# Kernel optimization log

Measured on AMD Instinct MI355X. Metric: run time of the kernel, lower is better.

## Reference

```python
import jax, jax.numpy as jnp
import numpy as np
from jax import lax

BETA = 10.0  # undeclared global softmax temperature in the source
STRIDE = 1
PADDING = 1


def setup_inputs() -> dict:
    key = jax.random.key(0)
    k1, k2 = jax.random.split(key)
    B, Ci, Co, K, L = 32, 256, 256, 3, 7  # num_level_conv=8 -> L=7
    x = jax.random.normal(k1, (B, Ci, 56, 56), dtype=jnp.float32)
    p_c = jax.random.normal(k2, (Co, Ci, K, K, L), dtype=jnp.float32)
    # reset_parameters with num_level=8, s=1: t1=4, t2=floor(log2(1))=0,
    # t3=arange(-2,1)=[-2,-1,0] -> q_level = sort(-2**t3) ++ [0] ++ 2**t3
    t3 = np.arange(-2, 1, dtype=np.float32)
    q_level = jnp.asarray(
        np.concatenate([np.sort(-(2.0 ** t3)), np.zeros(1, np.float32), 2.0 ** t3]),
        dtype=jnp.float32,
    )
    return {"x": x, "p_c": p_c, "q_level": q_level}


def reference(x, p_c, q_level):
    # soft quantization of the conv weight
    norm = jnp.sqrt(jnp.sum(p_c * p_c, axis=-1, keepdims=True))  # (O,I,K,K,1)
    s_c = jax.nn.softmax(BETA * (p_c / norm), axis=-1)           # (O,I,K,K,L)
    conv_w = jnp.einsum("oihwl,l->oihw", s_c, q_level)           # (O,I,K,K)
    # the source's double loop over (kh,kw) with strided slicing + matmul
    # is exactly stride-S cross-correlation with zero padding
    out = lax.conv_general_dilated(
        x,
        conv_w,
        window_strides=(STRIDE, STRIDE),
        padding=[(PADDING, PADDING), (PADDING, PADDING)],
        dimension_numbers=("NCHW", "OIHW", "NCHW"),
    )
    return out
```

## Files before the change

### kernel.cpp

```cpp
#include <hip/hip_runtime.h>
#include <math.h>

#define CI   256
#define CO   256
#define HW   56
#define LQ   7
#define BETA 10.0f

typedef __attribute__((ext_vector_type(8)))  short short8;
typedef __attribute__((ext_vector_type(16))) float f32x16;
typedef __attribute__((ext_vector_type(4)))  float f32x4;

__device__ __forceinline__ ushort f2bf(float f) {
    uint u = __float_as_uint(f);
    u += 0x7FFF + ((u >> 16) & 1);
    return (ushort)(u >> 16);
}

__global__ __launch_bounds__(256) void quant_weights(const float* __restrict__ p_c,
                                                     const float* __restrict__ q_level,
                                                     short* __restrict__ W2) {
    int idx = blockIdx.x * 256 + threadIdx.x;
    if (idx >= CO * CI * 9) return;
    int coci = idx / 9;
    int t = idx - coci * 9;
    int co = coci >> 8, ci = coci & 255;
    const float* p = p_c + (size_t)idx * LQ;
    float pv[LQ];
    float ss = 0.f;
#pragma unroll
    for (int l = 0; l < LQ; ++l) { pv[l] = p[l]; ss += pv[l] * pv[l]; }
    float inv = rsqrtf(ss) * BETA;
    float m = -1e30f;
#pragma unroll
    for (int l = 0; l < LQ; ++l) { pv[l] *= inv; m = fmaxf(m, pv[l]); }
    float den = 0.f, num = 0.f;
#pragma unroll
    for (int l = 0; l < LQ; ++l) {
        float e = expf(pv[l] - m);
        den += e;
        num += e * q_level[l];
    }
    int widx = ((((ci >> 5) * 9 + t) * 4 + ((ci >> 3) & 3)) * 2048) + co * 8 + (ci & 7);
    W2[widx] = (short)f2bf(num / den);
}

__global__ __launch_bounds__(256) void prep_main(const float* __restrict__ x,
                                                 ushort* __restrict__ xt) {
    __shared__ ushort ld[256 * 60];
    const int tid = threadIdx.x;
    const int h = blockIdx.x;
    const int b = blockIdx.y;

    if (h == 0 || h == 55) {
        int rr = (h == 0) ? 0 : 57;
        size_t base = ((size_t)b * 58 + rr) * 58 * 256;
        uint4 z = {0, 0, 0, 0};
        for (int i = tid; i < 58 * 256 / 8; i += 256)
            *(uint4*)&xt[base + (size_t)i * 8] = z;
    }
    if (tid < 64) {
        int col = (tid >> 5) * 57;
        int chk = tid & 31;
        size_t o = (((size_t)b * 58 + h + 1) * 58 + col) * 256 + chk * 8;
        uint4 z = {0, 0, 0, 0};
        *(uint4*)&xt[o] = z;
    }

    const float* xp = x + ((size_t)b * CI) * 3136 + h * HW;
#pragma unroll
    for (int s = 0; s < 14; ++s) {
        int flat = s * 1024 + tid * 4;
        int ci = flat / 56;
        int w  = flat - ci * 56;
        const float4 v = *(const float4*)(xp + (size_t)ci * 3136 + w);
        ushort4 o;
        o.x = f2bf(v.x); o.y = f2bf(v.y); o.z = f2bf(v.z); o.w = f2bf(v.w);
        *(ushort4*)&ld[ci * 60 + w] = o;
    }
    __syncthreads();
    const int w = tid & 63;
    const int wq = tid >> 6;
    if (w < 56) {
        size_t obase = (((size_t)b * 58 + h + 1) * 58 + (w + 1)) * 256;
#pragma unroll
        for (int s = 0; s < 8; ++s) {
            int cig = s * 4 + wq;
            int base = (cig * 8) * 60 + w;
            uint u0 = (uint)ld[base]       | ((uint)ld[base + 60]  << 16);
            uint u1 = (uint)ld[base + 120] | ((uint)ld[base + 180] << 16);
            uint u2 = (uint)ld[base + 240] | ((uint)ld[base + 300] << 16);
            uint u3 = (uint)ld[base + 360] | ((uint)ld[base + 420] << 16);
            uint4 o = {u0, u1, u2, u3};
            *(uint4*)&xt[obase + cig * 8] = o;
        }
    }
}

__global__ __launch_bounds__(256, 3) void conv_mfma3(const ushort* __restrict__ xt_g,
                                                     const short* __restrict__ W2,
                                                     float* __restrict__ out) {
    __shared__ __align__(16) ushort xt[2][8448];

    const int tid  = threadIdx.x;
    const int lane = tid & 63;
    const int wv   = tid >> 6;
    const int l31  = lane & 31;
    const int hi   = lane >> 5;
    const int wm   = (wv >> 1) * 64;
    const int wn   = wv & 1;

    const int h0  = blockIdx.x * 2;
    const int co0 = blockIdx.y * 128;
    const int b   = blockIdx.z;

    int src_off[5];
#pragma unroll
    for (int s = 0; s < 5; ++s) {
        int gl = s * 64 + lane;
        int g  = wv * 264 + (gl < 264 ? gl : 0);
        int kbq = g & 3, pos = g >> 2;
        int r = pos / 66, c = pos - r * 66;
        int cc = c < 58 ? c : 57;
        int cig = kbq ^ ((c >> 1) & 3);
        src_off[s] = ((b * 58 + h0 + r) * 58 + cc) * 256 + cig * 8;
    }

    f32x16 acc[2][2];
#pragma unroll
    for (int a = 0; a < 2; ++a)
#pragma unroll
        for (int f = 0; f < 2; ++f)
#pragma unroll
            for (int j = 0; j < 16; ++j) acc[a][f][j] = 0.f;

#pragma unroll
    for (int s = 0; s < 5; ++s) {
        if (s * 64 + lane < 264)
            __builtin_amdgcn_global_load_lds(
                (const __attribute__((address_space(1))) void*)(xt_g + src_off[s]),
                (__attribute__((address_space(3))) void*)&xt[0][(wv * 264 + s * 64) * 8],
                16, 0, 0);
    }

    for (int ch = 0; ch < 8; ++ch) {
        if (ch < 7) {
            const ushort* sp = xt_g + (ch + 1) * 32;
#pragma unroll
            for (int s = 0; s < 5; ++s) {
                if (s * 64 + lane < 264)
                    __builtin_amdgcn_global_load_lds(
                        (const __attribute__((address_space(1))) void*)(sp + src_off[s]),
                        (__attribute__((address_space(3))) void*)&xt[(ch + 1) & 1][(wv * 264 + s * 64) * 8],
                        16, 0, 0);
            }
            asm volatile("s_waitcnt vmcnt(5)" ::: "memory");
        } else {
            asm volatile("s_waitcnt vmcnt(0)" ::: "memory");
        }
        __builtin_amdgcn_s_barrier();

        const ushort* buf = xt[ch & 1];
#pragma unroll
        for (int kh = 0; kh < 3; ++kh) {
#pragma unroll
            for (int kw = 0; kw < 3; ++kw) {
                const int t = kh * 3 + kw;
#pragma unroll
                for (int k2 = 0; k2 < 2; ++k2) {
                    const int kb = k2 * 2 + hi;
                    const short* ap = W2 + (size_t)(((ch * 9 + t) * 4 + kb) * 256 + co0 + wm + l31) * 8;
                    short8 a0 = *(const short8*)ap;
                    short8 a1 = *(const short8*)(ap + 32 * 8);

                    const int c  = kw + l31;
                    const int r  = wn + kh;
                    const ushort* bp = &buf[((r * 66 + c) * 4 + (kb ^ ((c >> 1) & 3))) * 8];
                    short8 b0 = *(const short8*)bp;
                    short8 b1 = *(const short8*)(bp + 32 * 4 * 8);

                    acc[0][0] = __builtin_amdgcn_mfma_f32_32x32x16_bf16(a0, b0, acc[0][0], 0, 0, 0);
                    acc[0][1] = __builtin_amdgcn_mfma_f32_32x32x16_bf16(a0, b1, acc[0][1], 0, 0, 0);
                    acc[1][0] = __builtin_amdgcn_mfma_f32_32x32x16_bf16(a1, b0, acc[1][0], 0, 0, 0);
                    acc[1][1] = __builtin_amdgcn_mfma_f32_32x32x16_bf16(a1, b1, acc[1][1], 0, 0, 0);
                }
            }
        }
        asm volatile("s_waitcnt lgkmcnt(0)" ::: "memory");
        __builtin_amdgcn_s_barrier();
    }

    const int h = h0 + wn;
#pragma unroll
    for (int a = 0; a < 2; ++a) {
#pragma unroll
        for (int f = 0; f < 2; ++f) {
            int w = f * 32 + l31;
            if (w < HW) {
#pragma unroll
                for (int j = 0; j < 16; ++j) {
                    int co = co0 + wm + a * 32 + (j & 3) + 8 * (j >> 2) + 4 * hi;
                    out[(((size_t)b * CO + co) * HW + h) * HW + w] = acc[a][f][j];
                }
            }
        }
    }
}

__global__ __launch_bounds__(256, 2) void conv_mfma_fb(const float* __restrict__ x,
                                                       const short* __restrict__ W2,
                                                       float* __restrict__ out) {
    __shared__ __align__(16) short xs[6 * 72 * 32];

    const int tid  = threadIdx.x;
    const int lane = tid & 63;
    const int wv   = tid >> 6;
    const int l15  = lane & 15;
    const int kb   = lane >> 4;
    const int wm    = (wv >> 1) * 64;
    const int wnrow = (wv & 1) * 2;

    const int h0  = blockIdx.x * 4;
    const int co0 = blockIdx.y * 128;
    const int b   = blockIdx.z;

    f32x4 acc[4][8];
#pragma unroll
    for (int a = 0; a < 4; ++a)
#pragma unroll
        for (int f = 0; f < 8; ++f) acc[a][f] = (f32x4){0.f, 0.f, 0.f, 0.f};

    const float* xb = x + (size_t)b * CI * HW * HW;

    for (int ch = 0; ch < 8; ++ch) {
        const int ci0 = ch * 32;
        for (int f = tid; f < 6 * 66; f += 256) {
            int r = f / 66, c = f % 66;
            int h = h0 - 1 + r, wc = c - 1;
            bool valid = (h >= 0) & (h < HW) & (wc >= 0) & (wc < HW);
            const float* xsrc = xb + (size_t)ci0 * 3136 + (valid ? (h * HW + wc) : 0);
            int sw = (c >> 1) & 3;
            int sbase = (r * 72 + c) * 32;
#pragma unroll
            for (int k = 0; k < 4; ++k) {
                short8 pk;
#pragma unroll
                for (int e = 0; e < 8; ++e) {
                    float v = xsrc[(size_t)(k * 8 + e) * 3136];
                    pk[e] = (short)f2bf(valid ? v : 0.f);
                }
                *(short8*)&xs[sbase + ((k ^ sw) * 8)] = pk;
            }
        }
        __syncthreads();

#pragma unroll
        for (int kh = 0; kh < 3; ++kh) {
#pragma unroll
            for (int kw = 0; kw < 3; ++kw) {
                const int t = kh * 3 + kw;
                const short* ap = W2 + (size_t)((((ch * 9 + t) * 4 + kb) * 256) + co0 + wm + l15) * 8;
                short8 af[4];
#pragma unroll
                for (int a = 0; a < 4; ++a) af[a] = *(const short8*)(ap + a * 128);

                const int c0 = kw + l15;
                const int r0 = wnrow + kh;
                const short* bp = &xs[(r0 * 72 + c0) * 32 + ((kb ^ ((c0 >> 1) & 3)) * 8)];
                short8 bf[8];
#pragma unroll
                for (int f = 0; f < 8; ++f)
                    bf[f] = *(const short8*)(bp + (f >> 2) * 2304 + (f & 3) * 512);

#pragma unroll
                for (int a = 0; a < 4; ++a)
#pragma unroll
                    for (int f = 0; f < 8; ++f)
                        acc[a][f] = __builtin_amdgcn_mfma_f32_16x16x32_bf16(af[a], bf[f], acc[a][f], 0, 0, 0);
            }
        }
        __syncthreads();
    }

#pragma unroll
    for (int a = 0; a < 4; ++a) {
#pragma unroll
        for (int f = 0; f < 8; ++f) {
            int wloc = (f & 3) * 16 + l15;
            if (wloc < HW) {
                int h = h0 + wnrow + (f >> 2);
#pragma unroll
                for (int j = 0; j < 4; ++j) {
                    int cog = co0 + wm + 16 * a + kb * 4 + j;
                    out[(((size_t)b * CO + cog) * HW + h) * HW + wloc] = acc[a][f][j];
                }
            }
        }
    }
}

extern "C" void kernel_launch(void* const* d_in, const int* in_sizes, int n_in,
                              void* d_out, int out_size, void* d_ws, size_t ws_size,
                              hipStream_t stream) {
    const float* x       = (const float*)d_in[0];
    const float* p_c     = (const float*)d_in[1];
    const float* q_level = (const float*)d_in[2];
    float* out = (float*)d_out;

    short* W2 = (short*)d_ws;
    const size_t XT_OFF = 2u * 1024 * 1024;
    const size_t need = XT_OFF + (size_t)32 * 3364 * 256 * 2;

    quant_weights<<<(CO * CI * 9 + 255) / 256, 256, 0, stream>>>(p_c, q_level, W2);

    if (ws_size >= need) {
        ushort* xt_g = (ushort*)((char*)d_ws + XT_OFF);
        prep_main<<<dim3(56, 32), 256, 0, stream>>>(x, xt_g);
        conv_mfma3<<<dim3(28, 2, 32), 256, 0, stream>>>(xt_g, W2, out);
    } else {
        conv_mfma_fb<<<dim3(14, 2, 32), 256, 0, stream>>>(x, W2, out);
    }
}
```

Baseline: 196.7 us.

## Rewrite main conv kernel with 512-thread blocks, full Co tile, triple-buffered LDS

The main MFMA conv kernel becomes a 512-thread block that computes all 256 output channels for 4 output rows, instead of a 256-thread block covering 128 channels and 2 rows. It switches from 32x32x16 to 16x16x32 bf16 MFMAs with a 4x8 accumulator tile per wave. Input staging moves to a triple-buffered LDS ring, and the next tap's weight fragments are prefetched in registers, both meant to hide global latency and raise reuse of input and weights per block. In exchange it adds per-tap barriers, sets wave priority, raises register pressure, and launches half as many blocks.

```diff
diff --git a/kernel.cpp b/kernel.cpp
--- a/kernel.cpp
+++ b/kernel.cpp
@@ -8,7 +8,6 @@
 #define BETA 10.0f
 
 typedef __attribute__((ext_vector_type(8)))  short short8;
-typedef __attribute__((ext_vector_type(16))) float f32x16;
 typedef __attribute__((ext_vector_type(4)))  float f32x4;
 
 __device__ __forceinline__ ushort f2bf(float f) {
@@ -97,28 +96,26 @@
     }
 }
 
-__global__ __launch_bounds__(256, 3) void conv_mfma3(const ushort* __restrict__ xt_g,
+__global__ __launch_bounds__(512, 2) void conv_mfma8(const ushort* __restrict__ xt_g,
                                                      const short* __restrict__ W2,
                                                      float* __restrict__ out) {
-    __shared__ __align__(16) ushort xt[2][8448];
+    __shared__ __align__(16) ushort xt[3][12672];
 
     const int tid  = threadIdx.x;
     const int lane = tid & 63;
     const int wv   = tid >> 6;
-    const int l31  = lane & 31;
-    const int hi   = lane >> 5;
+    const int l15  = lane & 15;
+    const int kb   = lane >> 4;
     const int wm   = (wv >> 1) * 64;
-    const int wn   = wv & 1;
-
-    const int h0  = blockIdx.x * 2;
-    const int co0 = blockIdx.y * 128;
-    const int b   = blockIdx.z;
-
-    int src_off[5];
-#pragma unroll
-    for (int s = 0; s < 5; ++s) {
-        int gl = s * 64 + lane;
-        int g  = wv * 264 + (gl < 264 ? gl : 0);
+    const int wn   = (wv & 1) * 2;
+
+    const int h0 = blockIdx.x * 4;
+    const int b  = blockIdx.z;
+
+    int src_off[4];
+#pragma unroll
+    for (int s = 0; s < 4; ++s) {
+        int g = wv * 198 + s * 64 + lane;
         int kbq = g & 3, pos = g >> 2;
         int r = pos / 66, c = pos - r * 66;
         int cc = c < 58 ? c : 57;
@@ -126,85 +123,99 @@
         src_off[s] = ((b * 58 + h0 + r) * 58 + cc) * 256 + cig * 8;
     }
 
-    f32x16 acc[2][2];
-#pragma unroll
-    for (int a = 0; a < 2; ++a)
-#pragma unroll
-        for (int f = 0; f < 2; ++f)
-#pragma unroll
-            for (int j = 0; j < 16; ++j) acc[a][f][j] = 0.f;
-
-#pragma unroll
-    for (int s = 0; s < 5; ++s) {
-        if (s * 64 + lane < 264)
-            __builtin_amdgcn_global_load_lds(
-                (const __attribute__((address_space(1))) void*)(xt_g + src_off[s]),
-                (__attribute__((address_space(3))) void*)&xt[0][(wv * 264 + s * 64) * 8],
-                16, 0, 0);
-    }
+    f32x4 acc[4][8];
+#pragma unroll
+    for (int a = 0; a < 4; ++a)
+#pragma unroll
+        for (int f = 0; f < 8; ++f) acc[a][f] = (f32x4){0.f, 0.f, 0.f, 0.f};
+
+#define STAGE(CH2, S)                                                                \
+    if ((S) < 3 || lane < 6)                                                         \
+        __builtin_amdgcn_global_load_lds(                                            \
+            (const __attribute__((address_space(1))) void*)(xt_g + (CH2) * 32 + src_off[S]), \
+            (__attribute__((address_space(3))) void*)&xt[(CH2) % 3][(wv * 198 + (S) * 64) * 8], \
+            16, 0, 0)
+
+#define LOADA(DST, CH, T)                                                            \
+    {                                                                                \
+        const short* ap_ = W2 + (size_t)((((CH) * 9 + (T)) * 4 + kb) * 256 + wm + l15) * 8; \
+        DST[0] = *(const short8*)ap_;                                                \
+        DST[1] = *(const short8*)(ap_ + 128);                                        \
+        DST[2] = *(const short8*)(ap_ + 256);                                        \
+        DST[3] = *(const short8*)(ap_ + 384);                                        \
+    }
+
+    short8 afA[4], afB[4];
+
+#pragma unroll
+    for (int s = 0; s < 4; ++s) { STAGE(0, s); }
+#pragma unroll
+    for (int s = 0; s < 4; ++s) { STAGE(1, s); }
+    __builtin_amdgcn_sched_barrier(0);
+    LOADA(afA, 0, 0);
+    __builtin_amdgcn_sched_barrier(0);
+    asm volatile("s_waitcnt vmcnt(8)" ::: "memory");
+    __builtin_amdgcn_s_barrier();
 
     for (int ch = 0; ch < 8; ++ch) {
-        if (ch < 7) {
-            const ushort* sp = xt_g + (ch + 1) * 32;
-#pragma unroll
-            for (int s = 0; s < 5; ++s) {
-                if (s * 64 + lane < 264)
-                    __builtin_amdgcn_global_load_lds(
-                        (const __attribute__((address_space(1))) void*)(sp + src_off[s]),
-                        (__attribute__((address_space(3))) void*)&xt[(ch + 1) & 1][(wv * 264 + s * 64) * 8],
-                        16, 0, 0);
-            }
-            asm volatile("s_waitcnt vmcnt(5)" ::: "memory");
-        } else {
-            asm volatile("s_waitcnt vmcnt(0)" ::: "memory");
-        }
-        __builtin_amdgcn_s_barrier();
-
-        const ushort* buf = xt[ch & 1];
-#pragma unroll
-        for (int kh = 0; kh < 3; ++kh) {
-#pragma unroll
-            for (int kw = 0; kw < 3; ++kw) {
-                const int t = kh * 3 + kw;
-#pragma unroll
-                for (int k2 = 0; k2 < 2; ++k2) {
-                    const int kb = k2 * 2 + hi;
-                    const short* ap = W2 + (size_t)(((ch * 9 + t) * 4 + kb) * 256 + co0 + wm + l31) * 8;
-                    short8 a0 = *(const short8*)ap;
-                    short8 a1 = *(const short8*)(ap + 32 * 8);
-
-                    const int c  = kw + l31;
-                    const int r  = wn + kh;
-                    const ushort* bp = &buf[((r * 66 + c) * 4 + (kb ^ ((c >> 1) & 3))) * 8];
-                    short8 b0 = *(const short8*)bp;
-                    short8 b1 = *(const short8*)(bp + 32 * 4 * 8);
-
-                    acc[0][0] = __builtin_amdgcn_mfma_f32_32x32x16_bf16(a0, b0, acc[0][0], 0, 0, 0);
-                    acc[0][1] = __builtin_amdgcn_mfma_f32_32x32x16_bf16(a0, b1, acc[0][1], 0, 0, 0);
-                    acc[1][0] = __builtin_amdgcn_mfma_f32_32x32x16_bf16(a1, b0, acc[1][0], 0, 0, 0);
-                    acc[1][1] = __builtin_amdgcn_mfma_f32_32x32x16_bf16(a1, b1, acc[1][1], 0, 0, 0);
+        const ushort* buf = xt[ch % 3];
+#pragma unroll
+        for (int t = 0; t < 9; ++t) {
+            const int kh = t / 3, kw = t - kh * 3;
+            const int c0 = kw + l15;
+            const int r0 = wn + kh;
+            const ushort* bp = &buf[((r0 * 66 + c0) * 4 + (kb ^ ((c0 >> 1) & 3))) * 8];
+            short8 bf[8];
+#pragma unroll
+            for (int f = 0; f < 8; ++f)
+                bf[f] = *(const short8*)(bp + (f >> 2) * 2112 + (f & 3) * 512);
+
+            if (t < 8) {
+                LOADA(afB, ch, t + 1);
+            } else if (ch < 7) {
+                LOADA(afB, ch + 1, 0);
+            }
+            if (t < 4 && ch < 6) { STAGE(ch + 2, t); }
+            if (t == 8) {
+                if (ch < 6)       asm volatile("s_waitcnt vmcnt(8)" ::: "memory");
+                else if (ch == 6) asm volatile("s_waitcnt vmcnt(4)" ::: "memory");
+            }
+            __builtin_amdgcn_s_barrier();
+            asm volatile("s_waitcnt lgkmcnt(0)" ::: "memory");
+            __builtin_amdgcn_sched_barrier(0);
+
+            __builtin_amdgcn_s_setprio(1);
+#pragma unroll
+            for (int a = 0; a < 4; ++a)
+#pragma unroll
+                for (int f = 0; f < 8; ++f)
+                    acc[a][f] = __builtin_amdgcn_mfma_f32_16x16x32_bf16(afA[a], bf[f], acc[a][f], 0, 0, 0);
+            __builtin_amdgcn_s_setprio(0);
+            __builtin_amdgcn_s_barrier();
+
+            if (t < 8 || ch < 7) {
+                afA[0] = afB[0]; afA[1] = afB[1]; afA[2] = afB[2]; afA[3] = afB[3];
+            }
+        }
+    }
+
+#pragma unroll
+    for (int a = 0; a < 4; ++a) {
+#pragma unroll
+        for (int f = 0; f < 8; ++f) {
+            int wloc = (f & 3) * 16 + l15;
+            if (wloc < HW) {
+                int h = h0 + wn + (f >> 2);
+#pragma unroll
+                for (int j = 0; j < 4; ++j) {
+                    int cog = wm + 16 * a + kb * 4 + j;
+                    out[(((size_t)b * CO + cog) * HW + h) * HW + wloc] = acc[a][f][j];
                 }
             }
         }
-        asm volatile("s_waitcnt lgkmcnt(0)" ::: "memory");
-        __builtin_amdgcn_s_barrier();
-    }
-
-    const int h = h0 + wn;
-#pragma unroll
-    for (int a = 0; a < 2; ++a) {
-#pragma unroll
-        for (int f = 0; f < 2; ++f) {
-            int w = f * 32 + l31;
-            if (w < HW) {
-#pragma unroll
-                for (int j = 0; j < 16; ++j) {
-                    int co = co0 + wm + a * 32 + (j & 3) + 8 * (j >> 2) + 4 * hi;
-                    out[(((size_t)b * CO + co) * HW + h) * HW + w] = acc[a][f][j];
-                }
-            }
-        }
-    }
+    }
+#undef STAGE
+#undef LOADA
 }
 
 __global__ __launch_bounds__(256, 2) void conv_mfma_fb(const float* __restrict__ x,
@@ -316,7 +327,7 @@
     if (ws_size >= need) {
         ushort* xt_g = (ushort*)((char*)d_ws + XT_OFF);
         prep_main<<<dim3(56, 32), 256, 0, stream>>>(x, xt_g);
-        conv_mfma3<<<dim3(28, 2, 32), 256, 0, stream>>>(xt_g, W2, out);
+        conv_mfma8<<<dim3(14, 1, 32), 512, 0, stream>>>(xt_g, W2, out);
     } else {
         conv_mfma_fb<<<dim3(14, 2, 32), 256, 0, stream>>>(x, W2, out);
     }
```

New measurement: 254.9 us. 1.3x slower.

## Retile conv to 4 rows x 64 channels per block with one row per wave

Applied to the files above, without the earlier changes.

Each block of the main MFMA conv now covers 4 output rows and 64 output channels instead of 2 rows and 128 channels. Each wave owns one output row across all 64 channels. The input tile in LDS grows to 6 rows in a kb-major layout without the XOR swizzle, and each tap issues 8 MFMAs covering both K halves, with s_setprio raised around them. Input halo reuse improves and weight traffic per output changes. The cost is a larger LDS footprint, a stricter vmcnt(0) wait at the end of every chunk, and possible LDS bank conflicts now that the swizzle is gone.

```diff
diff --git a/kernel.cpp b/kernel.cpp
--- a/kernel.cpp
+++ b/kernel.cpp
@@ -8,14 +8,19 @@
 #define BETA 10.0f
 
 typedef __attribute__((ext_vector_type(8)))  short short8;
+typedef __attribute__((ext_vector_type(4)))  float f32x4;
 typedef __attribute__((ext_vector_type(16))) float f32x16;
-typedef __attribute__((ext_vector_type(4)))  float f32x4;
 
 __device__ __forceinline__ ushort f2bf(float f) {
     uint u = __float_as_uint(f);
     u += 0x7FFF + ((u >> 16) & 1);
     return (ushort)(u >> 16);
 }
+
+#define GLDS(SRC, DST)                                                        \
+    __builtin_amdgcn_global_load_lds(                                         \
+        (const __attribute__((address_space(1))) void*)(SRC),                 \
+        (__attribute__((address_space(3))) void*)(DST), 16, 0, 0)
 
 __global__ __launch_bounds__(256) void quant_weights(const float* __restrict__ p_c,
                                                      const float* __restrict__ q_level,
@@ -97,33 +102,30 @@
     }
 }
 
-__global__ __launch_bounds__(256, 3) void conv_mfma3(const ushort* __restrict__ xt_g,
-                                                     const short* __restrict__ W2,
-                                                     float* __restrict__ out) {
-    __shared__ __align__(16) ushort xt[2][8448];
+__global__ __launch_bounds__(256, 3) void conv32(const ushort* __restrict__ xt_g,
+                                                 const short* __restrict__ W2,
+                                                 float* __restrict__ out) {
+    __shared__ __align__(16) ushort Bb[2][12672];
 
     const int tid  = threadIdx.x;
     const int lane = tid & 63;
     const int wv   = tid >> 6;
     const int l31  = lane & 31;
     const int hi   = lane >> 5;
-    const int wm   = (wv >> 1) * 64;
-    const int wn   = wv & 1;
-
-    const int h0  = blockIdx.x * 2;
-    const int co0 = blockIdx.y * 128;
+
+    const int h0  = blockIdx.x * 4;
+    const int co0 = blockIdx.y * 64;
     const int b   = blockIdx.z;
 
-    int src_off[5];
-#pragma unroll
-    for (int s = 0; s < 5; ++s) {
+    int bsrc[7];
+#pragma unroll
+    for (int s = 0; s < 7; ++s) {
         int gl = s * 64 + lane;
-        int g  = wv * 264 + (gl < 264 ? gl : 0);
-        int kbq = g & 3, pos = g >> 2;
-        int r = pos / 66, c = pos - r * 66;
+        int g  = wv * 396 + (gl < 396 ? gl : 0);
+        int r = g / 264, rem = g - r * 264;
+        int kbq = rem / 66, c = rem - kbq * 66;
         int cc = c < 58 ? c : 57;
-        int cig = kbq ^ ((c >> 1) & 3);
-        src_off[s] = ((b * 58 + h0 + r) * 58 + cc) * 256 + cig * 8;
+        bsrc[s] = ((b * 58 + h0 + r) * 58 + cc) * 256 + kbq * 8;
     }
 
     f32x16 acc[2][2];
@@ -134,63 +136,57 @@
 #pragma unroll
             for (int j = 0; j < 16; ++j) acc[a][f][j] = 0.f;
 
-#pragma unroll
-    for (int s = 0; s < 5; ++s) {
-        if (s * 64 + lane < 264)
-            __builtin_amdgcn_global_load_lds(
-                (const __attribute__((address_space(1))) void*)(xt_g + src_off[s]),
-                (__attribute__((address_space(3))) void*)&xt[0][(wv * 264 + s * 64) * 8],
-                16, 0, 0);
-    }
+#define STAGE(CH)                                                     \
+    {                                                                 \
+        const ushort* sp_ = xt_g + (CH) * 32;                         \
+        ushort* lb_ = &Bb[(CH) & 1][wv * 396 * 8];                    \
+        _Pragma("unroll")                                             \
+        for (int s_ = 0; s_ < 7; ++s_)                                \
+            if (s_ * 64 + lane < 396)                                 \
+                GLDS(sp_ + bsrc[s_], lb_ + s_ * 512);                 \
+    }
+
+    STAGE(0);
+    asm volatile("s_waitcnt vmcnt(0)" ::: "memory");
+    __builtin_amdgcn_s_barrier();
 
     for (int ch = 0; ch < 8; ++ch) {
-        if (ch < 7) {
-            const ushort* sp = xt_g + (ch + 1) * 32;
-#pragma unroll
-            for (int s = 0; s < 5; ++s) {
-                if (s * 64 + lane < 264)
-                    __builtin_amdgcn_global_load_lds(
-                        (const __attribute__((address_space(1))) void*)(sp + src_off[s]),
-                        (__attribute__((address_space(3))) void*)&xt[(ch + 1) & 1][(wv * 264 + s * 64) * 8],
-                        16, 0, 0);
-            }
-            asm volatile("s_waitcnt vmcnt(5)" ::: "memory");
-        } else {
-            asm volatile("s_waitcnt vmcnt(0)" ::: "memory");
-        }
+        if (ch < 7) STAGE(ch + 1);
+        const ushort* buf = Bb[ch & 1];
+        const short* wp = W2 + (size_t)(ch * 9 * 4 * 256) * 8 + (size_t)(hi * 256 + co0 + l31) * 8;
+#pragma unroll
+        for (int t = 0; t < 9; ++t) {
+            const int kh = t / 3, kw = t - kh * 3;
+            short8 a00 = *(const short8*)(wp);
+            short8 a01 = *(const short8*)(wp + 32 * 8);
+            short8 a10 = *(const short8*)(wp + 2 * 256 * 8);
+            short8 a11 = *(const short8*)(wp + 2 * 256 * 8 + 32 * 8);
+
+            const int gb = ((wv + kh) * 4 + hi) * 66 + kw + l31;
+            short8 b00 = *(const short8*)&buf[(size_t)gb * 8];
+            short8 b01 = *(const short8*)&buf[(size_t)(gb + 32) * 8];
+            short8 b10 = *(const short8*)&buf[(size_t)(gb + 132) * 8];
+            short8 b11 = *(const short8*)&buf[(size_t)(gb + 164) * 8];
+
+            __builtin_amdgcn_s_setprio(1);
+            acc[0][0] = __builtin_amdgcn_mfma_f32_32x32x16_bf16(a00, b00, acc[0][0], 0, 0, 0);
+            acc[0][1] = __builtin_amdgcn_mfma_f32_32x32x16_bf16(a00, b01, acc[0][1], 0, 0, 0);
+            acc[1][0] = __builtin_amdgcn_mfma_f32_32x32x16_bf16(a01, b00, acc[1][0], 0, 0, 0);
+            acc[1][1] = __builtin_amdgcn_mfma_f32_32x32x16_bf16(a01, b01, acc[1][1], 0, 0, 0);
+            acc[0][0] = __builtin_amdgcn_mfma_f32_32x32x16_bf16(a10, b10, acc[0][0], 0, 0, 0);
+            acc[0][1] = __builtin_amdgcn_mfma_f32_32x32x16_bf16(a10, b11, acc[0][1], 0, 0, 0);
+            acc[1][0] = __builtin_amdgcn_mfma_f32_32x32x16_bf16(a11, b10, acc[1][0], 0, 0, 0);
+            acc[1][1] = __builtin_amdgcn_mfma_f32_32x32x16_bf16(a11, b11, acc[1][1], 0, 0, 0);
+            __builtin_amdgcn_s_setprio(0);
+
+            wp += 4 * 256 * 8;
+        }
+        asm volatile("s_waitcnt vmcnt(0) lgkmcnt(0)" ::: "memory");
         __builtin_amdgcn_s_barrier();
-
-        const ushort* buf = xt[ch & 1];
-#pragma unroll
-        for (int kh = 0; kh < 3; ++kh) {
-#pragma unroll
-            for (int kw = 0; kw < 3; ++kw) {
-                const int t = kh * 3 + kw;
-#pragma unroll
-                for (int k2 = 0; k2 < 2; ++k2) {
-                    const int kb = k2 * 2 + hi;
-                    const short* ap = W2 + (size_t)(((ch * 9 + t) * 4 + kb) * 256 + co0 + wm + l31) * 8;
-                    short8 a0 = *(const short8*)ap;
-                    short8 a1 = *(const short8*)(ap + 32 * 8);
-
-                    const int c  = kw + l31;
-                    const int r  = wn + kh;
-                    const ushort* bp = &buf[((r * 66 + c) * 4 + (kb ^ ((c >> 1) & 3))) * 8];
-                    short8 b0 = *(const short8*)bp;
-                    short8 b1 = *(const short8*)(bp + 32 * 4 * 8);
-
-                    acc[0][0] = __builtin_amdgcn_mfma_f32_32x32x16_bf16(a0, b0, acc[0][0], 0, 0, 0);
-                    acc[0][1] = __builtin_amdgcn_mfma_f32_32x32x16_bf16(a0, b1, acc[0][1], 0, 0, 0);
-                    acc[1][0] = __builtin_amdgcn_mfma_f32_32x32x16_bf16(a1, b0, acc[1][0], 0, 0, 0);
-                    acc[1][1] = __builtin_amdgcn_mfma_f32_32x32x16_bf16(a1, b1, acc[1][1], 0, 0, 0);
-                }
-            }
-        }
-        asm volatile("s_waitcnt lgkmcnt(0)" ::: "memory");
-        __builtin_amdgcn_s_barrier();
-    }
-
-    const int h = h0 + wn;
+    }
+#undef STAGE
+
+    const int h = h0 + wv;
 #pragma unroll
     for (int a = 0; a < 2; ++a) {
 #pragma unroll
@@ -199,7 +195,7 @@
             if (w < HW) {
 #pragma unroll
                 for (int j = 0; j < 16; ++j) {
-                    int co = co0 + wm + a * 32 + (j & 3) + 8 * (j >> 2) + 4 * hi;
+                    int co = co0 + a * 32 + (j & 3) + 8 * (j >> 2) + 4 * hi;
                     out[(((size_t)b * CO + co) * HW + h) * HW + w] = acc[a][f][j];
                 }
             }
@@ -316,7 +312,7 @@
     if (ws_size >= need) {
         ushort* xt_g = (ushort*)((char*)d_ws + XT_OFF);
         prep_main<<<dim3(56, 32), 256, 0, stream>>>(x, xt_g);
-        conv_mfma3<<<dim3(28, 2, 32), 256, 0, stream>>>(xt_g, W2, out);
+        conv32<<<dim3(14, 4, 32), 256, 0, stream>>>(xt_g, W2, out);
     } else {
         conv_mfma_fb<<<dim3(14, 2, 32), 256, 0, stream>>>(x, W2, out);
     }
```

Result: slower. 217.6 us (+10.7%).
